# Kernel tuning notes

Measured on AMD Instinct MI355X. Metric: run time of the kernel, lower is better.

The kernel has to match this reference:

```python
import jax, jax.numpy as jnp
import numpy as np

B, T, E = 2, 2048, 1024
H = 16
D = E // H  # head_dim = 64


def setup_inputs() -> dict:
    key = jax.random.key(0)
    ks = jax.random.split(key, 9)
    s = 1.0 / np.sqrt(E)
    inp = {"x": jax.random.normal(ks[0], (B, T, E), dtype=jnp.float32)}
    # Linear params (torch nn.Linear: y = x @ W.T + b)
    inp["Wq"] = jax.random.uniform(ks[1], (E, E), jnp.float32, -s, s)
    inp["bq"] = jax.random.uniform(ks[2], (E,), jnp.float32, -s, s)
    inp["Wk"] = jax.random.uniform(ks[3], (E, E), jnp.float32, -s, s)
    inp["bk"] = jax.random.uniform(ks[4], (E,), jnp.float32, -s, s)
    inp["Wv"] = jax.random.uniform(ks[5], (E, E), jnp.float32, -s, s)
    inp["bv"] = jax.random.uniform(ks[6], (E,), jnp.float32, -s, s)
    inp["Wo"] = jax.random.uniform(ks[7], (E, E), jnp.float32, -s, s)
    inp["bo"] = jax.random.uniform(ks[8], (E,), jnp.float32, -s, s)
    return inp


def reference(x, Wq, bq, Wk, bk, Wv, bv, Wo, bo):
    # QKV projections, reshape to [B, H, T, D]
    def split_heads(y):
        return y.reshape(B, T, H, D).transpose(0, 2, 1, 3)

    Q = split_heads(x @ Wq.T + bq)
    K = split_heads(x @ Wk.T + bk)
    V = split_heads(x @ Wv.T + bv)

    scale = 1.0 / jnp.sqrt(jnp.asarray(D, x.dtype))
    scores = jnp.einsum("bhqd,bhkd->bhqk", Q, K) * scale  # [B,H,T,T]
    attn = jax.nn.softmax(scores, axis=-1)
    out = jnp.einsum("bhqk,bhkd->bhqd", attn, V)  # [B,H,T,D]
    out = out.transpose(0, 2, 1, 3).reshape(B, T, E)
    # dropout is identity in eval mode
    return out @ Wo.T + bo
```

## Files before the change

### kernel.cpp

```cpp
#include <hip/hip_runtime.h>
#include <math.h>

#define BB 2
#define TT 2048
#define EE 1024
#define HH 16
#define DD 64
#define MM (BB*TT)
#define KK EE

typedef short bf16x8 __attribute__((ext_vector_type(8)));
typedef float f32x4  __attribute__((ext_vector_type(4)));

__device__ __forceinline__ unsigned short f2bf(float f) {
  unsigned int u = __float_as_uint(f);
  u = (u + 0x7FFFu + ((u >> 16) & 1u)) >> 16;
  return (unsigned short)u;
}

__device__ __forceinline__ void async16(const void* g, void* l) {
  __builtin_amdgcn_global_load_lds(
      (const __attribute__((address_space(1))) unsigned int*)g,
      (__attribute__((address_space(3))) unsigned int*)l, 16, 0, 0);
}

__global__ __launch_bounds__(256) void to_bf16(
    const float* __restrict__ x,  const float* __restrict__ wq,
    const float* __restrict__ wk, const float* __restrict__ wv,
    const float* __restrict__ wo,
    unsigned short* __restrict__ xh, unsigned short* __restrict__ wcat,
    unsigned short* __restrict__ woh)
{
  int c = blockIdx.x * 256 + threadIdx.x;
  const float* src; unsigned short* dst; int off;
  if (c < 1048576) { src = x; dst = xh; off = c; }
  else {
    int r = c - 1048576;
    int w = r >> 18;
    off = r & 262143;
    if      (w == 0) { src = wq; dst = wcat; }
    else if (w == 1) { src = wk; dst = wcat + (1 << 20); }
    else if (w == 2) { src = wv; dst = wcat + (2 << 20); }
    else             { src = wo; dst = woh; }
  }
  float4 v = ((const float4*)src)[off];
  ushort4 h;
  h.x = f2bf(v.x); h.y = f2bf(v.y); h.z = f2bf(v.z); h.w = f2bf(v.w);
  ((ushort4*)dst)[off] = h;
}

template<int MODE>
__global__ __launch_bounds__(512) void gemm_bf16(
    const unsigned short* __restrict__ A, const unsigned short* __restrict__ B,
    const float* __restrict__ b0p, const float* __restrict__ b1p,
    const float* __restrict__ b2p,
    unsigned short* __restrict__ oq, unsigned short* __restrict__ ok,
    unsigned short* __restrict__ ov, float* __restrict__ ofp, float qscale)
{
  constexpr int NT = (MODE == 0) ? 128 : 64;
  constexpr int JN = NT / 32;
  constexpr int BROWS = NT * 32;
  constexpr int TOT = (MODE == 0) ? 16 : 12;
  __shared__ unsigned short S[(MODE == 0) ? 17408 : 12288];

  const int tid  = threadIdx.x;
  const int lane = tid & 63;
  const int wv   = tid >> 6;
  const int col  = lane & 15;
  const int quad = lane >> 4;
  const int wm = (wv & 3) * 32;
  const int wn = (wv >> 2) * (NT / 2);
  const int m0 = blockIdx.x * 128;
  const int n0 = blockIdx.y * NT;

  const int srow = lane >> 2;
  const int sw16 = (((lane & 3) ^ ((lane >> 2) & 3)) << 3);
  const int fswA = ((quad ^ (col & 3)) << 3);

  auto stage = [&](int kt, int b) {
#pragma unroll
    for (int s = 0; s < 2; ++s) {
      const int t = wv * 2 + s;
      if (t < TOT) {
        const unsigned short* src; int rb, g0, loff;
        if (t < 8) { src = A; rb = t * 16;       g0 = m0; loff = b * 4096; }
        else       { src = B; rb = (t - 8) * 16; g0 = n0; loff = 8192 + b * BROWS; }
        async16(src + (size_t)(g0 + rb + srow) * KK + kt + sw16,
                S + loff + rb * 32);
      }
    }
  };

  f32x4 acc[2][JN];
  const f32x4 z = {0.f, 0.f, 0.f, 0.f};
#pragma unroll
  for (int i = 0; i < 2; ++i)
#pragma unroll
    for (int j = 0; j < JN; ++j) acc[i][j] = z;

  stage(0, 0);
  __syncthreads();

  for (int kt = 0; kt < KK; kt += 32) {
    const int buf = (kt >> 5) & 1;
    if (kt + 32 < KK) stage(kt + 32, buf ^ 1);

    const unsigned short* Asb = S + buf * 4096;
    const unsigned short* Bsb = S + 8192 + buf * BROWS;
    bf16x8 bf[JN];
#pragma unroll
    for (int j = 0; j < JN; ++j)
      bf[j] = *(const bf16x8*)(Bsb + (wn + j * 16 + col) * 32 + fswA);
#pragma unroll
    for (int i = 0; i < 2; ++i) {
      bf16x8 af = *(const bf16x8*)(Asb + (wm + i * 16 + col) * 32 + fswA);
#pragma unroll
      for (int j = 0; j < JN; ++j)
        acc[i][j] = __builtin_amdgcn_mfma_f32_16x16x32_bf16(af, bf[j], acc[i][j], 0, 0, 0);
    }
    __syncthreads();
  }

  unsigned short* Cs = S;
  if (MODE == 0) {
    const int region = n0 >> 10;
    const float* bias = (region == 0) ? b0p : (region == 1) ? b1p : b2p;
    const float scl = (region == 0) ? qscale : 1.0f;
    const int nlbase = n0 & 1023;
    const int h0 = nlbase >> 6;
    const int b = m0 >> 11, t0 = m0 & (TT - 1);
    if (region < 2) {
#pragma unroll
      for (int i = 0; i < 2; ++i)
#pragma unroll
        for (int j = 0; j < 4; ++j) {
          const int nt = wn + j * 16 + col;
          const float bs = bias[nlbase + nt];
#pragma unroll
          for (int r = 0; r < 4; ++r) {
            const int mt = wm + i * 16 + quad * 4 + r;
            Cs[mt * 136 + nt] = f2bf((acc[i][j][r] + bs) * scl);
          }
        }
      __syncthreads();
      unsigned short* dst = (region == 0) ? oq : ok;
#pragma unroll
      for (int s = 0; s < 4; ++s) {
        const int u = s * 512 + tid;
        const int mt = u >> 4, hs = (u >> 3) & 1, ch = u & 7;
        const size_t g = ((size_t)(b * HH + h0 + hs) * TT + t0 + mt) * DD + ch * 8;
        *(uint4*)(dst + g) = *(const uint4*)(Cs + mt * 136 + hs * 64 + ch * 8);
      }
    } else {
#pragma unroll
      for (int i = 0; i < 2; ++i)
#pragma unroll
        for (int j = 0; j < 4; ++j) {
          const int nt = wn + j * 16 + col;
          const float bs = bias[nlbase + nt];
          ushort4 pk;
          pk.x = f2bf(acc[i][j][0] + bs);
          pk.y = f2bf(acc[i][j][1] + bs);
          pk.z = f2bf(acc[i][j][2] + bs);
          pk.w = f2bf(acc[i][j][3] + bs);
          *(ushort4*)(Cs + nt * 136 + wm + i * 16 + quad * 4) = pk;
        }
      __syncthreads();
#pragma unroll
      for (int s = 0; s < 4; ++s) {
        const int u = s * 512 + tid;
        const int nt = u >> 4, ch = u & 15;
        const int d = nt & 63, hs = nt >> 6;
        const size_t g = ((size_t)(b * HH + h0 + hs) * DD + d) * TT + t0 + ch * 8;
        *(uint4*)(ov + g) = *(const uint4*)(Cs + nt * 136 + ch * 8);
      }
    }
  } else {
#pragma unroll
    for (int i = 0; i < 2; ++i) {
#pragma unroll
      for (int j = 0; j < JN; ++j) {
        const int n = n0 + wn + j * 16 + col;
        const float bs = b0p[n];
#pragma unroll
        for (int r = 0; r < 4; ++r) {
          const int m = m0 + wm + i * 16 + quad * 4 + r;
          ofp[(size_t)m * EE + n] = acc[i][j][r] + bs;
        }
      }
    }
  }
}

__global__ __launch_bounds__(512, 4) void flash_mfma(
    const unsigned short* __restrict__ Qb, const unsigned short* __restrict__ Kb,
    const unsigned short* __restrict__ Vtb, unsigned short* __restrict__ ctx)
{
  __shared__ unsigned short QPs[128 * 72];
  __shared__ unsigned short Ks[2][64 * 64];
  __shared__ unsigned short Vts[2][64 * 64];

  const int tid  = threadIdx.x;
  const int lane = tid & 63;
  const int wv   = tid >> 6;
  const int col  = lane & 15;
  const int quad = lane >> 4;
  const int wm   = wv * 16;
  const int gid  = blockIdx.x;
  const int bh   = gid & 31;
  const int q0   = (gid >> 5) * 128;

  const unsigned short* Qg = Qb  + (size_t)bh * TT * DD;
  const unsigned short* Kg = Kb  + (size_t)bh * TT * DD;
  const unsigned short* Vg = Vtb + (size_t)bh * DD * TT;

  const int srow = lane >> 3;
  const int sw16 = (((lane & 7) ^ ((lane >> 3) & 7)) << 3);
  const int cxor = (col & 7);

  const int rbK = (wv & 3) * 16;
  const bool isK = (wv < 4);
  const unsigned short* g0 =
      (isK ? Kg + (size_t)(rbK + srow) * DD : Vg + (size_t)(rbK + srow) * TT) + sw16;
  const unsigned short* g1 = g0 + (isK ? 8 * DD : 8 * TT);
  unsigned short* l0 = (isK ? &Ks[0][0] : &Vts[0][0]) + rbK * 64;
  unsigned short* l1 = l0 + 8 * 64;
  const int gstep = isK ? 64 * DD : 64;

  auto stage_kv = [&](int ti, int b) {
    const size_t go = (size_t)ti * gstep;
    async16(g0 + go, l0 + b * 4096);
    async16(g1 + go, l1 + b * 4096);
  };

  int kvo[4][2];
#pragma unroll
  for (int j = 0; j < 4; ++j)
#pragma unroll
    for (int h = 0; h < 2; ++h)
      kvo[j][h] = ((j * 16 + col) * 64 + (((h * 4 + quad) ^ cxor) << 3)) * 2;
  const int prow  = (wm + col) * 72;
  const int pwo   = (prow + quad * 4) * 2;
  const int pro0  = (prow + quad * 8) * 2;
  const int pro1  = (prow + 32 + quad * 8) * 2;

#pragma unroll
  for (int s = 0; s < 2; ++s) {
    const int rb = wv * 16 + s * 8;
    async16(Qg + (size_t)(q0 + rb + srow) * DD + sw16, &QPs[rb * 64]);
  }
  stage_kv(0, 0);
  __syncthreads();

  bf16x8 aq[2];
#pragma unroll
  for (int h = 0; h < 2; ++h)
    aq[h] = *(const bf16x8*)(QPs + (wm + col) * 64 +
                             (((h * 4 + quad) ^ cxor) << 3));
  __syncthreads();

  f32x4 o_acc[4];
  float lpart = 0.f;
  const f32x4 z = {0.f, 0.f, 0.f, 0.f};
#pragma unroll
  for (int j = 0; j < 4; ++j) o_acc[j] = z;

#define KV_TILE(KT, BUF) do {                                                 \
    if ((KT) + 64 < TT) stage_kv(((KT) >> 6) + 1, (BUF) ^ 1);                 \
    const char* Kp = (const char*)&Ks[BUF][0];                                \
    const char* Vp = (const char*)&Vts[BUF][0];                               \
    f32x4 sacc[4];                                                            \
    _Pragma("unroll")                                                         \
    for (int j = 0; j < 4; ++j) sacc[j] = z;                                  \
    __builtin_amdgcn_s_setprio(1);                                            \
    _Pragma("unroll")                                                         \
    for (int j = 0; j < 4; ++j) {                                             \
      bf16x8 bk0 = *(const bf16x8*)(Kp + kvo[j][0]);                          \
      bf16x8 bk1 = *(const bf16x8*)(Kp + kvo[j][1]);                          \
      sacc[j] = __builtin_amdgcn_mfma_f32_16x16x32_bf16(bk0, aq[0], sacc[j], 0, 0, 0); \
      sacc[j] = __builtin_amdgcn_mfma_f32_16x16x32_bf16(bk1, aq[1], sacc[j], 0, 0, 0); \
    }                                                                         \
    __builtin_amdgcn_s_setprio(0);                                            \
    {                                                                         \
      float lp0 = 0.f, lp1 = 0.f;                                             \
      _Pragma("unroll")                                                       \
      for (int j = 0; j < 4; ++j) {                                           \
        float p0 = __builtin_amdgcn_exp2f(sacc[j][0]);                        \
        float p1 = __builtin_amdgcn_exp2f(sacc[j][1]);                        \
        float p2 = __builtin_amdgcn_exp2f(sacc[j][2]);                        \
        float p3 = __builtin_amdgcn_exp2f(sacc[j][3]);                        \
        lp0 += p0 + p1; lp1 += p2 + p3;                                       \
        uint2 w;                                                              \
        w.x = __builtin_amdgcn_perm(__float_as_uint(p1), __float_as_uint(p0), 0x07060302u); \
        w.y = __builtin_amdgcn_perm(__float_as_uint(p3), __float_as_uint(p2), 0x07060302u); \
        *(uint2*)((char*)QPs + pwo + j * 32) = w;                             \
      }                                                                       \
      lpart += lp0 + lp1;                                                     \
    }                                                                         \
    bf16x8 ap0 = *(const bf16x8*)((const char*)QPs + pro0);                   \
    bf16x8 ap1 = *(const bf16x8*)((const char*)QPs + pro1);                   \
    __builtin_amdgcn_s_setprio(1);                                            \
    _Pragma("unroll")                                                         \
    for (int j = 0; j < 4; ++j) {                                             \
      bf16x8 bv0 = *(const bf16x8*)(Vp + kvo[j][0]);                          \
      bf16x8 bv1 = *(const bf16x8*)(Vp + kvo[j][1]);                          \
      o_acc[j] = __builtin_amdgcn_mfma_f32_16x16x32_bf16(ap0, bv0, o_acc[j], 0, 0, 0); \
      o_acc[j] = __builtin_amdgcn_mfma_f32_16x16x32_bf16(ap1, bv1, o_acc[j], 0, 0, 0); \
    }                                                                         \
    __builtin_amdgcn_s_setprio(0);                                            \
    __syncthreads();                                                          \
  } while (0)

  for (int kt = 0; kt < TT; kt += 128) {
    KV_TILE(kt, 0);
    KV_TILE(kt + 64, 1);
  }
#undef KV_TILE

  unsigned short* Cs = &Ks[0][0];
  const int b = bh >> 4, h = bh & 15;
  float l = lpart;
  l += __shfl_xor(l, 16);
  l += __shfl_xor(l, 32);
#pragma unroll
  for (int r = 0; r < 4; ++r) {
    const float inv = 1.0f / __shfl(l, quad * 4 + r);
    const int trow = wm + quad * 4 + r;
#pragma unroll
    for (int j = 0; j < 4; ++j) {
      const int n = j * 16 + col;
      const int ch = ((n >> 3) ^ (trow & 7)) << 3;
      Cs[trow * 64 + ch + (n & 7)] = f2bf(o_acc[j][r] * inv);
    }
  }
  __syncthreads();
#pragma unroll
  for (int s = 0; s < 2; ++s) {
    const int u = s * 512 + tid;
    const int mr = u >> 3, ch = u & 7;
    const size_t g = ((size_t)(b * TT + q0 + mr)) * EE + h * DD + ch * 8;
    const int chs = (ch ^ (mr & 7)) << 3;
    *(uint4*)(ctx + g) = *(const uint4*)(Cs + mr * 64 + chs);
  }
}

extern "C" void kernel_launch(void* const* d_in, const int* in_sizes, int n_in,
                              void* d_out, int out_size, void* d_ws, size_t ws_size,
                              hipStream_t stream) {
  const float* x  = (const float*)d_in[0];
  const float* Wq = (const float*)d_in[1];
  const float* bq = (const float*)d_in[2];
  const float* Wk = (const float*)d_in[3];
  const float* bk = (const float*)d_in[4];
  const float* Wv = (const float*)d_in[5];
  const float* bv = (const float*)d_in[6];
  const float* Wo = (const float*)d_in[7];
  const float* bo = (const float*)d_in[8];

  unsigned short* p = (unsigned short*)d_ws;
  const size_t XN = (size_t)MM * EE;
  const size_t WN = (size_t)EE * EE;
  unsigned short* x_h    = p;           p += XN;
  unsigned short* Wcat_h = p;           p += 3 * WN;
  unsigned short* Wo_h   = p;           p += WN;
  unsigned short* Qb     = p;           p += XN;
  unsigned short* Kb     = p;           p += XN;
  unsigned short* Vtb    = p;           p += XN;
  unsigned short* ctx_h  = x_h;

  to_bf16<<<8192, 256, 0, stream>>>(x, Wq, Wk, Wv, Wo, x_h, Wcat_h, Wo_h);

  const float qscale = 0.125f * 1.44269504088896f;

  gemm_bf16<0><<<dim3(MM / 128, 3 * EE / 128), 512, 0, stream>>>(
      x_h, Wcat_h, bq, bk, bv, Qb, Kb, Vtb, nullptr, qscale);

  flash_mfma<<<dim3((TT / 128) * BB * HH), 512, 0, stream>>>(Qb, Kb, Vtb, ctx_h);

  gemm_bf16<2><<<dim3(MM / 128, EE / 64), 512, 0, stream>>>(
      ctx_h, Wo_h, bo, nullptr, nullptr,
      nullptr, nullptr, nullptr, (float*)d_out, 1.0f);
}
```

Baseline: 187.8 us.

## Triple-buffer K/V tiles and software-pipeline QK^T one tile ahead of PV

```diff
diff --git a/kernel.cpp b/kernel.cpp
--- a/kernel.cpp
+++ b/kernel.cpp
@@ -197,8 +197,8 @@
     const unsigned short* __restrict__ Vtb, unsigned short* __restrict__ ctx)
 {
   __shared__ unsigned short QPs[128 * 72];
-  __shared__ unsigned short Ks[2][64 * 64];
-  __shared__ unsigned short Vts[2][64 * 64];
+  __shared__ unsigned short Ks[3][64 * 64];
+  __shared__ unsigned short Vts[3][64 * 64];
 
   const int tid  = threadIdx.x;
   const int lane = tid & 63;
@@ -227,10 +227,10 @@
   unsigned short* l1 = l0 + 8 * 64;
   const int gstep = isK ? 64 * DD : 64;
 
-  auto stage_kv = [&](int ti, int b) {
+  auto stage_kv = [&](int ti, int slot) {
     const size_t go = (size_t)ti * gstep;
-    async16(g0 + go, l0 + b * 4096);
-    async16(g1 + go, l1 + b * 4096);
+    async16(g0 + go, l0 + slot * 4096);
+    async16(g1 + go, l1 + slot * 4096);
   };
 
   int kvo[4][2];
@@ -250,6 +250,7 @@
     async16(Qg + (size_t)(q0 + rb + srow) * DD + sw16, &QPs[rb * 64]);
   }
   stage_kv(0, 0);
+  stage_kv(1, 1);
   __syncthreads();
 
   bf16x8 aq[2];
@@ -259,29 +260,32 @@
                              (((h * 4 + quad) ^ cxor) << 3));
   __syncthreads();
 
-  f32x4 o_acc[4];
+  f32x4 o_acc[4], sacc[4], nsacc[4];
   float lpart = 0.f;
   const f32x4 z = {0.f, 0.f, 0.f, 0.f};
 #pragma unroll
   for (int j = 0; j < 4; ++j) o_acc[j] = z;
 
-#define KV_TILE(KT, BUF) do {                                                 \
-    if ((KT) + 64 < TT) stage_kv(((KT) >> 6) + 1, (BUF) ^ 1);                 \
-    const char* Kp = (const char*)&Ks[BUF][0];                                \
-    const char* Vp = (const char*)&Vts[BUF][0];                               \
-    f32x4 sacc[4];                                                            \
-    _Pragma("unroll")                                                         \
-    for (int j = 0; j < 4; ++j) sacc[j] = z;                                  \
-    __builtin_amdgcn_s_setprio(1);                                            \
-    _Pragma("unroll")                                                         \
-    for (int j = 0; j < 4; ++j) {                                             \
-      bf16x8 bk0 = *(const bf16x8*)(Kp + kvo[j][0]);                          \
-      bf16x8 bk1 = *(const bf16x8*)(Kp + kvo[j][1]);                          \
-      sacc[j] = __builtin_amdgcn_mfma_f32_16x16x32_bf16(bk0, aq[0], sacc[j], 0, 0, 0); \
-      sacc[j] = __builtin_amdgcn_mfma_f32_16x16x32_bf16(bk1, aq[1], sacc[j], 0, 0, 0); \
-    }                                                                         \
-    __builtin_amdgcn_s_setprio(0);                                            \
-    {                                                                         \
+  {
+    const char* Kp = (const char*)&Ks[0][0];
+#pragma unroll
+    for (int j = 0; j < 4; ++j) sacc[j] = z;
+#pragma unroll
+    for (int j = 0; j < 4; ++j) {
+      bf16x8 bk0 = *(const bf16x8*)(Kp + kvo[j][0]);
+      bf16x8 bk1 = *(const bf16x8*)(Kp + kvo[j][1]);
+      sacc[j] = __builtin_amdgcn_mfma_f32_16x16x32_bf16(bk0, aq[0], sacc[j], 0, 0, 0);
+      sacc[j] = __builtin_amdgcn_mfma_f32_16x16x32_bf16(bk1, aq[1], sacc[j], 0, 0, 0);
+    }
+  }
+
+#define BODY(T, B0, B1, B2, DOSTAGE, DOQK, VMC) do {                          \
+    if (DOSTAGE) stage_kv((T) + 2, B2);                                       \
+    asm volatile("s_waitcnt vmcnt(" #VMC ")" ::: "memory");                   \
+    __builtin_amdgcn_sched_barrier(0);                                        \
+    __builtin_amdgcn_s_barrier();                                             \
+    __builtin_amdgcn_sched_barrier(0);                                        \
+    {            \
       float lp0 = 0.f, lp1 = 0.f;                                             \
       _Pragma("unroll")                                                       \
       for (int j = 0; j < 4; ++j) {                                           \
@@ -297,25 +301,52 @@
       }                                                                       \
       lpart += lp0 + lp1;                                                     \
     }                                                                         \
-    bf16x8 ap0 = *(const bf16x8*)((const char*)QPs + pro0);                   \
-    bf16x8 ap1 = *(const bf16x8*)((const char*)QPs + pro1);                   \
-    __builtin_amdgcn_s_setprio(1);                                            \
-    _Pragma("unroll")                                                         \
-    for (int j = 0; j < 4; ++j) {                                             \
-      bf16x8 bv0 = *(const bf16x8*)(Vp + kvo[j][0]);                          \
-      bf16x8 bv1 = *(const bf16x8*)(Vp + kvo[j][1]);                          \
-      o_acc[j] = __builtin_amdgcn_mfma_f32_16x16x32_bf16(ap0, bv0, o_acc[j], 0, 0, 0); \
-      o_acc[j] = __builtin_amdgcn_mfma_f32_16x16x32_bf16(ap1, bv1, o_acc[j], 0, 0, 0); \
+    if (DOQK) {      \
+      const char* Kp = (const char*)&Ks[B1][0];                               \
+      _Pragma("unroll")                                                       \
+      for (int j = 0; j < 4; ++j) nsacc[j] = z;                               \
+      __builtin_amdgcn_s_setprio(1);                                          \
+      _Pragma("unroll")                                                       \
+      for (int j = 0; j < 4; ++j) {                                           \
+        bf16x8 bk0 = *(const bf16x8*)(Kp + kvo[j][0]);                        \
+        bf16x8 bk1 = *(const bf16x8*)(Kp + kvo[j][1]);                        \
+        nsacc[j] = __builtin_amdgcn_mfma_f32_16x16x32_bf16(bk0, aq[0], nsacc[j], 0, 0, 0); \
+        nsacc[j] = __builtin_amdgcn_mfma_f32_16x16x32_bf16(bk1, aq[1], nsacc[j], 0, 0, 0); \
+      }                                                                       \
+      __builtin_amdgcn_s_setprio(0);                                          \
     }                                                                         \
-    __builtin_amdgcn_s_setprio(0);                                            \
-    __syncthreads();                                                          \
+    {                                                              \
+      bf16x8 ap0 = *(const bf16x8*)((const char*)QPs + pro0);                 \
+      bf16x8 ap1 = *(const bf16x8*)((const char*)QPs + pro1);                 \
+      const char* Vp = (const char*)&Vts[B0][0];                              \
+      __builtin_amdgcn_s_setprio(1);                                          \
+      _Pragma("unroll")                                                       \
+      for (int j = 0; j < 4; ++j) {                                           \
+        bf16x8 bv0 = *(const bf16x8*)(Vp + kvo[j][0]);                        \
+        bf16x8 bv1 = *(const bf16x8*)(Vp + kvo[j][1]);                        \
+        o_acc[j] = __builtin_amdgcn_mfma_f32_16x16x32_bf16(ap0, bv0, o_acc[j], 0, 0, 0); \
+        o_acc[j] = __builtin_amdgcn_mfma_f32_16x16x32_bf16(ap1, bv1, o_acc[j], 0, 0, 0); \
+      }                                                                       \
+      __builtin_amdgcn_s_setprio(0);                                          \
+    }                                                                         \
+    asm volatile("s_waitcnt lgkmcnt(0)" ::: "memory");                        \
+    __builtin_amdgcn_sched_barrier(0);                                        \
+    __builtin_amdgcn_s_barrier();                                             \
+    __builtin_amdgcn_sched_barrier(0);                                        \
+    if (DOQK) {                                                               \
+      _Pragma("unroll")                                                       \
+      for (int j = 0; j < 4; ++j) sacc[j] = nsacc[j];                         \
+    }                                                                         \
   } while (0)
 
-  for (int kt = 0; kt < TT; kt += 128) {
-    KV_TILE(kt, 0);
-    KV_TILE(kt + 64, 1);
-  }
-#undef KV_TILE
+  for (int t = 0; t < 30; t += 3) {
+    BODY(t,     0, 1, 2, 1, 1, 2);
+    BODY(t + 1, 1, 2, 0, 1, 1, 2);
+    BODY(t + 2, 2, 0, 1, 1, 1, 2);
+  }
+  BODY(30, 0, 1, 2, 0, 1, 0);
+  BODY(31, 1, 2, 0, 0, 0, 0);
+#undef BODY
 
   unsigned short* Cs = &Ks[0][0];
   const int b = bh >> 4, h = bh & 15;
```

Measured after the change: 186.6 us. Within noise of the previous version (-0.6%).
